# Optimization experiments

Hardware: AMD Instinct MI355X
Metric: run time of the kernel (lower is better)

## Reference

```python
import jax, jax.numpy as jnp
import numpy as np

DIM = 2048
DIM_VISUAL = 1024
HEADS = 16
DIM_HEAD = 64
INNER = HEADS * DIM_HEAD  # 1024
EPS = 1e-5


def setup_inputs() -> dict:
    key = jax.random.key(0)
    ks = jax.random.split(key, 6)
    y = jax.random.normal(ks[0], (4, 2048, DIM), dtype=jnp.float32)
    visual_features = jax.random.normal(ks[1], (4, 8, 64, DIM_VISUAL), dtype=jnp.float32)
    ln_g = jnp.ones((DIM,), dtype=jnp.float32)
    ln_b = jnp.zeros((DIM,), dtype=jnp.float32)
    Wq = jax.random.normal(ks[2], (DIM, INNER), dtype=jnp.float32) * 0.02
    Wkv = jax.random.normal(ks[3], (DIM_VISUAL, 2 * INNER), dtype=jnp.float32) * 0.02
    Wo = jax.random.normal(ks[4], (INNER, DIM), dtype=jnp.float32) * 0.02
    return {"y": y, "visual_features": visual_features, "ln_g": ln_g, "ln_b": ln_b,
            "Wq": Wq, "Wkv": Wkv, "Wo": Wo}


def reference(y, visual_features, ln_g, ln_b, Wq, Wkv, Wo):
    scale = DIM_HEAD ** (-0.5)
    b, t, nq, dv = visual_features.shape
    # LayerNorm over last dim
    mu = jnp.mean(y, axis=-1, keepdims=True)
    var = jnp.mean(jnp.square(y - mu), axis=-1, keepdims=True)
    yn = (y - mu) * jax.lax.rsqrt(var + EPS) * ln_g + ln_b
    q = (yn @ Wq) * scale                      # (b, n, inner)
    vis = visual_features.reshape(b, t * nq, dv)
    kv = vis @ Wkv                             # (b, m, 2*inner)
    k, v = jnp.split(kv, 2, axis=-1)
    # split heads: b n (h d) -> b h n d
    split = lambda x: x.reshape(x.shape[0], x.shape[1], HEADS, DIM_HEAD).transpose(0, 2, 1, 3)
    q, k, v = split(q), split(k), split(v)
    sim = jnp.einsum('bhid,bhjd->bhij', q, k)
    alphas = jax.nn.softmax(sim, axis=-1)      # amax-subtract softmax (stable)
    out = jnp.einsum('bhij,bhjd->bhid', alphas, v)
    out = out.transpose(0, 2, 1, 3).reshape(out.shape[0], out.shape[2], INNER)
    return out @ Wo
```

## Files before the change

### kernel.cpp

```cpp
#include <hip/hip_runtime.h>
#include <stdint.h>

typedef unsigned short u16;
typedef __bf16 bfrag __attribute__((ext_vector_type(8)));
typedef float f32x4 __attribute__((ext_vector_type(4)));
typedef u16 u16x4 __attribute__((ext_vector_type(4)));

__device__ __forceinline__ float bf2f(u16 u) {
  union { unsigned i; float f; } x; x.i = ((unsigned)u) << 16; return x.f;
}
__device__ __forceinline__ u16 f2bf(float f) {
  union { unsigned i; float f; } x; x.f = f;
  unsigned r = x.i + 0x7fffu + ((x.i >> 16) & 1u);
  return (u16)(r >> 16);
}
__device__ __forceinline__ unsigned packbf(float lo, float hi) {
  return (unsigned)f2bf(lo) | ((unsigned)f2bf(hi) << 16);
}

__device__ __forceinline__ f32x4 mfma16(bfrag a, bfrag b, f32x4 c) {
  return __builtin_amdgcn_mfma_f32_16x16x32_bf16(a, b, c, 0, 0, 0);
}

__device__ __forceinline__ void gl_lds16(const u16* g, const u16* l) {
  __builtin_amdgcn_global_load_lds(
      (const __attribute__((address_space(1))) unsigned int*)g,
      (__attribute__((address_space(3))) unsigned int*)l, 16, 0, 0);
}

__device__ __forceinline__ void xcd_swizzle(int& bx, int& by) {
  int gx = gridDim.x, nwg = gx * gridDim.y;
  int flat = by * gx + bx;
  int cpx = nwg >> 3;
  int swz = (flat & 7) * cpx + (flat >> 3);
  bx = swz % gx;
  by = swz / gx;
}

__global__ __launch_bounds__(256) void k_transpose(const float* __restrict__ in,
                                                   u16* __restrict__ out, int R, int C) {
  __shared__ u16 tile[32][33];
  int c0 = blockIdx.x * 32, r0 = blockIdx.y * 32;
  int tx = threadIdx.x, ty = threadIdx.y;
#pragma unroll
  for (int i = 0; i < 4; ++i)
    tile[ty + i * 8][tx] = f2bf(in[(size_t)(r0 + ty + i * 8) * C + c0 + tx]);
  __syncthreads();
#pragma unroll
  for (int i = 0; i < 4; ++i)
    out[(size_t)(c0 + ty + i * 8) * R + r0 + tx] = tile[tx][ty + i * 8];
}

__global__ __launch_bounds__(256) void k_cast(const float* __restrict__ in,
                                              u16* __restrict__ out, int n8) {
  int i = blockIdx.x * 256 + threadIdx.x;
  if (i >= n8) return;
  float4 a = *(const float4*)(in + (size_t)i * 8);
  float4 b = *(const float4*)(in + (size_t)i * 8 + 4);
  uint4 ov; u16* po = (u16*)&ov;
  po[0] = f2bf(a.x); po[1] = f2bf(a.y); po[2] = f2bf(a.z); po[3] = f2bf(a.w);
  po[4] = f2bf(b.x); po[5] = f2bf(b.y); po[6] = f2bf(b.z); po[7] = f2bf(b.w);
  *(uint4*)(out + (size_t)i * 8) = ov;
}

__global__ __launch_bounds__(256) void k_layernorm(const float* __restrict__ y,
                                                   const float* __restrict__ g,
                                                   const float* __restrict__ bb,
                                                   u16* __restrict__ yn) {
  int row = blockIdx.x, t = threadIdx.x;
  const float* yr = y + (size_t)row * 2048 + t * 8;
  float4 v0 = *(const float4*)(yr);
  float4 v1 = *(const float4*)(yr + 4);
  float x[8] = {v0.x, v0.y, v0.z, v0.w, v1.x, v1.y, v1.z, v1.w};
  float s = 0.f, ss = 0.f;
#pragma unroll
  for (int j = 0; j < 8; ++j) { s += x[j]; ss += x[j] * x[j]; }
#pragma unroll
  for (int off = 32; off > 0; off >>= 1) {
    s += __shfl_down(s, off);
    ss += __shfl_down(ss, off);
  }
  __shared__ float rs[4], rq[4];
  int lane = t & 63, wid = t >> 6;
  if (lane == 0) { rs[wid] = s; rq[wid] = ss; }
  __syncthreads();
  float S = rs[0] + rs[1] + rs[2] + rs[3];
  float Q = rq[0] + rq[1] + rq[2] + rq[3];
  float mean = S * (1.f / 2048.f);
  float var = Q * (1.f / 2048.f) - mean * mean;
  float rstd = rsqrtf(var + 1e-5f);
  float4 g0 = *(const float4*)(g + t * 8);
  float4 g1 = *(const float4*)(g + t * 8 + 4);
  float4 b0 = *(const float4*)(bb + t * 8);
  float4 b1 = *(const float4*)(bb + t * 8 + 4);
  float gg[8] = {g0.x, g0.y, g0.z, g0.w, g1.x, g1.y, g1.z, g1.w};
  float bv[8] = {b0.x, b0.y, b0.z, b0.w, b1.x, b1.y, b1.z, b1.w};
  uint4 ov; u16* po = (u16*)&ov;
#pragma unroll
  for (int j = 0; j < 8; ++j)
    po[j] = f2bf((x[j] - mean) * rstd * gg[j] + bv[j]);
  *(uint4*)(yn + (size_t)row * 2048 + t * 8) = ov;
}

template <bool F32OUT>
__global__ __launch_bounds__(256) void k_gemm_bt(const u16* __restrict__ A,
                                                 const u16* __restrict__ Bt,
                                                 void* __restrict__ Cv,
                                                 int M, int N, int K, float scale) {
  __shared__ __align__(16) u16 As[128 * 64];
  __shared__ __align__(16) u16 Bs[128 * 64];
  int t = threadIdx.x, lane = t & 63, wid = t >> 6;
  int wm = wid >> 1, wn = wid & 1;
  int bx = blockIdx.x, by = blockIdx.y;
  xcd_swizzle(bx, by);
  int m0 = by * 128, n0 = bx * 128;
  int lr = lane & 15, lg = lane >> 4;
  int sk = lr & 7;

  f32x4 acc[4][4];
#pragma unroll
  for (int i = 0; i < 4; ++i)
#pragma unroll
    for (int j = 0; j < 4; ++j) acc[i][j] = (f32x4){0.f, 0.f, 0.f, 0.f};

  int srow[4], scol[4], sbase[4];
#pragma unroll
  for (int j = 0; j < 4; ++j) {
    int s0 = (wid * 4 + j) * 64;
    int s = s0 + lane;
    srow[j] = s >> 3;
    scol[j] = ((s & 7) ^ (srow[j] & 7)) * 8;
    sbase[j] = s0 * 8;
  }

  for (int k0 = 0; k0 < K; k0 += 64) {
#pragma unroll
    for (int j = 0; j < 4; ++j) {
      gl_lds16(A + (size_t)(m0 + srow[j]) * K + k0 + scol[j], As + sbase[j]);
      gl_lds16(Bt + (size_t)(n0 + srow[j]) * K + k0 + scol[j], Bs + sbase[j]);
    }
    __syncthreads();
#pragma unroll
    for (int kk = 0; kk < 2; ++kk) {
      bfrag a[4], b[4];
#pragma unroll
      for (int i = 0; i < 4; ++i)
        a[i] = *(const bfrag*)(As + (wm * 64 + i * 16 + lr) * 64 + (((kk * 4 + lg) ^ sk) * 8));
#pragma unroll
      for (int j = 0; j < 4; ++j)
        b[j] = *(const bfrag*)(Bs + (wn * 64 + j * 16 + lr) * 64 + (((kk * 4 + lg) ^ sk) * 8));
#pragma unroll
      for (int i = 0; i < 4; ++i)
#pragma unroll
        for (int j = 0; j < 4; ++j)
          acc[i][j] = mfma16(a[i], b[j], acc[i][j]);
    }
    __syncthreads();
  }
#pragma unroll
  for (int i = 0; i < 4; ++i)
#pragma unroll
    for (int j = 0; j < 4; ++j) {
      int r0 = m0 + wm * 64 + i * 16 + lg * 4;
      int c0 = n0 + wn * 64 + j * 16 + lr;
#pragma unroll
      for (int r = 0; r < 4; ++r) {
        float v = scale * acc[i][j][r];
        if (F32OUT)
          ((float*)Cv)[(size_t)(r0 + r) * N + c0] = v;
        else
          ((u16*)Cv)[(size_t)(r0 + r) * N + c0] = f2bf(v);
      }
    }
}

__global__ __launch_bounds__(256) void k_gemm_kv(const u16* __restrict__ A,
                                                 const u16* __restrict__ Bt,
                                                 u16* __restrict__ Kb,
                                                 u16* __restrict__ Vtb) {
  const int K = 1024;
  __shared__ __align__(16) u16 As[128 * 64];
  __shared__ __align__(16) u16 Bs[128 * 64];
  int t = threadIdx.x, lane = t & 63, wid = t >> 6;
  int wm = wid >> 1, wn = wid & 1;
  int bx = blockIdx.x, by = blockIdx.y;
  xcd_swizzle(bx, by);
  int m0 = by * 128, n0 = bx * 128;
  int lr = lane & 15, lg = lane >> 4;
  int sk = lr & 7;

  f32x4 acc[4][4];
#pragma unroll
  for (int i = 0; i < 4; ++i)
#pragma unroll
    for (int j = 0; j < 4; ++j) acc[i][j] = (f32x4){0.f, 0.f, 0.f, 0.f};

  int srow[4], scol[4], sbase[4];
#pragma unroll
  for (int j = 0; j < 4; ++j) {
    int s0 = (wid * 4 + j) * 64;
    int s = s0 + lane;
    srow[j] = s >> 3;
    scol[j] = ((s & 7) ^ (srow[j] & 7)) * 8;
    sbase[j] = s0 * 8;
  }

  for (int k0 = 0; k0 < K; k0 += 64) {
#pragma unroll
    for (int j = 0; j < 4; ++j) {
      gl_lds16(A + (size_t)(m0 + srow[j]) * K + k0 + scol[j], As + sbase[j]);
      gl_lds16(Bt + (size_t)(n0 + srow[j]) * K + k0 + scol[j], Bs + sbase[j]);
    }
    __syncthreads();
#pragma unroll
    for (int kk = 0; kk < 2; ++kk) {
      bfrag a[4], b[4];
#pragma unroll
      for (int i = 0; i < 4; ++i)
        a[i] = *(const bfrag*)(As + (wm * 64 + i * 16 + lr) * 64 + (((kk * 4 + lg) ^ sk) * 8));
#pragma unroll
      for (int j = 0; j < 4; ++j)
        b[j] = *(const bfrag*)(Bs + (wn * 64 + j * 16 + lr) * 64 + (((kk * 4 + lg) ^ sk) * 8));
#pragma unroll
      for (int i = 0; i < 4; ++i)
#pragma unroll
        for (int j = 0; j < 4; ++j)
          acc[i][j] = mfma16(a[i], b[j], acc[i][j]);
    }
    __syncthreads();
  }
#pragma unroll
  for (int i = 0; i < 4; ++i)
#pragma unroll
    for (int j = 0; j < 4; ++j) {
      int r0 = m0 + wm * 64 + i * 16 + lg * 4;
      int c0 = n0 + wn * 64 + j * 16 + lr;
      if (c0 < 1024) {
#pragma unroll
        for (int r = 0; r < 4; ++r)
          Kb[(size_t)(r0 + r) * 1024 + c0] = f2bf(acc[i][j][r]);
      } else {
        int d = c0 - 1024;
        int hh = d >> 6, dd = d & 63;
        int bq = r0 >> 9, kvp = r0 & 511;
        u16x4 pk;
#pragma unroll
        for (int r = 0; r < 4; ++r) pk[r] = f2bf(acc[i][j][r]);
        *(u16x4*)(Vtb + ((size_t)(bq * 16 + hh) * 64 + dd) * 512 + kvp) = pk;
      }
    }
}

__global__ __launch_bounds__(256, 2) void k_attn(const u16* __restrict__ q,
                                                 const u16* __restrict__ kb,
                                                 const u16* __restrict__ vt,
                                                 u16* __restrict__ ao) {
  __shared__ __align__(16) u16 Ks[128 * 64];
  __shared__ __align__(16) u16 Vt[64 * 128];
  int t = threadIdx.x, lane = t & 63, wid = t >> 6;
  int lr = lane & 15, lg = lane >> 4;
  int sk = lr & 7;
  int a_ = lg >> 1, b_ = lg & 1;
  int bh = blockIdx.y, b = bh >> 4, h = bh & 15;
  int q0 = blockIdx.x * 128 + wid * 32;

  const u16* qg = q + (size_t)(b * 2048 + q0) * 1024 + h * 64;
  bfrag qf[2][2];
#pragma unroll
  for (int rt = 0; rt < 2; ++rt)
#pragma unroll
    for (int kk = 0; kk < 2; ++kk)
      qf[rt][kk] = *(const bfrag*)(qg + (size_t)(rt * 16 + lr) * 1024 + kk * 32 + lg * 8);

  f32x4 o[2][4];
#pragma unroll
  for (int rt = 0; rt < 2; ++rt)
#pragma unroll
    for (int dt = 0; dt < 4; ++dt) o[rt][dt] = (f32x4){0.f, 0.f, 0.f, 0.f};
  float m_s[2] = {-1e30f, -1e30f}, l_s[2] = {0.f, 0.f};

  const u16* kgb = kb + (size_t)(b * 512) * 1024 + h * 64;
  const u16* vgb = vt + (size_t)bh * 64 * 512;

  int krow[4], kcol[4], kbase[4];
#pragma unroll
  for (int j = 0; j < 4; ++j) {
    int g = wid * 4 + j;
    int s = g * 64 + lane;
    krow[j] = s >> 3;
    kcol[j] = ((s & 7) ^ (krow[j] & 7)) * 8;
    kbase[j] = g * 512;
  }

  for (int it = 0; it < 4; ++it) {
    int kv0 = it * 128;
#pragma unroll
    for (int j = 0; j < 4; ++j)
      gl_lds16(kgb + (size_t)(kv0 + krow[j]) * 1024 + kcol[j], Ks + kbase[j]);
#pragma unroll
    for (int j = 0; j < 4; ++j) {
      int g = wid * 4 + j;
      int d = g * 4 + (lane >> 4);
      int p = lane & 15;
      gl_lds16(vgb + (size_t)d * 512 + kv0 + ((p ^ (d & 7)) * 8), Vt + g * 512);
    }
    __syncthreads();

#pragma unroll
    for (int rt = 0; rt < 2; ++rt) {
      f32x4 s[8];
#pragma unroll
      for (int ct = 0; ct < 8; ++ct) {
        s[ct] = (f32x4){0.f, 0.f, 0.f, 0.f};
#pragma unroll
        for (int kk = 0; kk < 2; ++kk) {
          bfrag kf = *(const bfrag*)(Ks + (ct * 16 + lr) * 64 + (((kk * 4 + lg) ^ sk) * 8));
          s[ct] = mfma16(kf, qf[rt][kk], s[ct]);
        }
      }
      float mloc = -1e30f;
#pragma unroll
      for (int ct = 0; ct < 8; ++ct)
#pragma unroll
        for (int r = 0; r < 4; ++r) mloc = fmaxf(mloc, s[ct][r]);
      mloc = fmaxf(mloc, __shfl_xor(mloc, 16));
      mloc = fmaxf(mloc, __shfl_xor(mloc, 32));
      float mn = fmaxf(m_s[rt], mloc);
      float scq = __expf(m_s[rt] - mn);
      float ps = 0.f;
#pragma unroll
      for (int ct = 0; ct < 8; ++ct)
#pragma unroll
        for (int r = 0; r < 4; ++r) {
          float p = __expf(s[ct][r] - mn);
          s[ct][r] = p;
          ps += p;
        }
      ps += __shfl_xor(ps, 16);
      ps += __shfl_xor(ps, 32);
      l_s[rt] = l_s[rt] * scq + ps;
      m_s[rt] = mn;
      float sc4[4];
#pragma unroll
      for (int r = 0; r < 4; ++r) sc4[r] = __shfl(scq, (lane & 48) | (lg * 4 + r));
#pragma unroll
      for (int dt = 0; dt < 4; ++dt)
#pragma unroll
        for (int r = 0; r < 4; ++r) o[rt][dt][r] *= sc4[r];

      unsigned w0[8], w1[8];
#pragma unroll
      for (int ct = 0; ct < 8; ++ct) {
        w0[ct] = packbf(s[ct][0], s[ct][1]);
        w1[ct] = packbf(s[ct][2], s[ct][3]);
      }
      bfrag pf[4];
#pragma unroll
      for (int kt = 0; kt < 4; ++kt) {
        unsigned c0w0 = w0[2 * kt], c0w1 = w1[2 * kt];
        unsigned c1w0 = w0[2 * kt + 1], c1w1 = w1[2 * kt + 1];
        unsigned s0 = a_ ? c0w0 : c1w0;
        unsigned s1 = a_ ? c0w1 : c1w1;
        unsigned k0 = a_ ? c1w0 : c0w0;
        unsigned k1 = a_ ? c1w1 : c0w1;
        unsigned r0 = (unsigned)__shfl_xor((int)s0, 32);
        unsigned r1 = (unsigned)__shfl_xor((int)s1, 32);
        unsigned x0 = (a_ == b_) ? r0 : k0;
        unsigned x1 = (a_ == b_) ? r1 : k1;
        unsigned kk0 = (a_ == b_) ? k0 : r0;
        unsigned kk1 = (a_ == b_) ? k1 : r1;
        unsigned q0_ = (unsigned)__shfl_xor((int)x0, 16);
        unsigned q1_ = (unsigned)__shfl_xor((int)x1, 16);
        union { unsigned u[4]; bfrag f; } uf;
        uf.u[0] = b_ ? q0_ : kk0;
        uf.u[1] = b_ ? q1_ : kk1;
        uf.u[2] = b_ ? kk0 : q0_;
        uf.u[3] = b_ ? kk1 : q1_;
        pf[kt] = uf.f;
      }
#pragma unroll
      for (int dt = 0; dt < 4; ++dt)
#pragma unroll
        for (int kt = 0; kt < 4; ++kt) {
          int d = dt * 16 + lr;
          bfrag vfb = *(const bfrag*)(Vt + d * 128 + (((kt * 4 + lg) ^ (d & 7)) * 8));
          o[rt][dt] = mfma16(pf[kt], vfb, o[rt][dt]);
        }
    }
    __syncthreads();
  }

#pragma unroll
  for (int rt = 0; rt < 2; ++rt) {
    float invq = 1.f / l_s[rt];
    float i4[4];
#pragma unroll
    for (int r = 0; r < 4; ++r) i4[r] = __shfl(invq, (lane & 48) | (lg * 4 + r));
#pragma unroll
    for (int dt = 0; dt < 4; ++dt)
#pragma unroll
      for (int r = 0; r < 4; ++r)
        ao[(size_t)(b * 2048 + q0 + rt * 16 + lg * 4 + r) * 1024 + h * 64 + dt * 16 + lr] =
            f2bf(o[rt][dt][r] * i4[r]);
  }
}

extern "C" void kernel_launch(void* const* d_in, const int* in_sizes, int n_in,
                              void* d_out, int out_size, void* d_ws, size_t ws_size,
                              hipStream_t stream) {
  const float* y   = (const float*)d_in[0];
  const float* vf  = (const float*)d_in[1];
  const float* g   = (const float*)d_in[2];
  const float* bb  = (const float*)d_in[3];
  const float* Wq  = (const float*)d_in[4];
  const float* Wkv = (const float*)d_in[5];
  const float* Wo  = (const float*)d_in[6];
  float* out = (float*)d_out;
  char* ws = (char*)d_ws;

  u16* qb   = (u16*)(ws + 0ull);
  u16* kbuf = (u16*)(ws + 16777216ull);
  u16* vtb  = (u16*)(ws + 20971520ull);
  u16* aob  = (u16*)(ws + 25165824ull);
  u16* wqT  = (u16*)(ws + 41943040ull);
  u16* wkvT = (u16*)(ws + 46137344ull);
  u16* woT  = (u16*)(ws + 50331648ull);
  u16* vfb  = (u16*)(ws + 54525952ull);
  u16* yn = (u16*)d_out;

  dim3 tb(32, 8, 1);
  k_transpose<<<dim3(1024 / 32, 2048 / 32, 1), tb, 0, stream>>>(Wq, wqT, 2048, 1024);
  k_transpose<<<dim3(2048 / 32, 1024 / 32, 1), tb, 0, stream>>>(Wkv, wkvT, 1024, 2048);
  k_transpose<<<dim3(2048 / 32, 1024 / 32, 1), tb, 0, stream>>>(Wo, woT, 1024, 2048);
  k_cast<<<(2048 * 1024 / 8 + 255) / 256, 256, 0, stream>>>(vf, vfb, 2048 * 1024 / 8);
  k_layernorm<<<8192, 256, 0, stream>>>(y, g, bb, yn);
  k_gemm_bt<false><<<dim3(1024 / 128, 8192 / 128, 1), 256, 0, stream>>>(yn, wqT, qb, 8192, 1024, 2048, 0.125f);
  k_gemm_kv<<<dim3(2048 / 128, 2048 / 128, 1), 256, 0, stream>>>(vfb, wkvT, kbuf, vtb);
  k_attn<<<dim3(16, 64, 1), 256, 0, stream>>>(qb, kbuf, vtb, aob);
  k_gemm_bt<true><<<dim3(2048 / 128, 8192 / 128, 1), 256, 0, stream>>>(aob, woT, out, 8192, 2048, 1024, 1.0f);
}
```

Before: 189.2 us.

## Double-buffer LDS tiles in GEMM and attention kernels to overlap loads

Adds a second LDS buffer for the A/B tiles in both GEMM kernels and for the K/V tiles in the attention kernel. The next tile's global-to-LDS copy is issued before computing on the current tile, with one barrier per iteration. The aim is to hide global load latency behind the MFMA work. It doubles LDS use per block (64KB for the GEMMs, 64KB for attention at 2 blocks/CU), which may reduce occupancy. The loop now has a single barrier per step, so correctness depends on gl_lds16 completion being covered by __syncthreads.

```diff
diff --git a/kernel.cpp b/kernel.cpp
--- a/kernel.cpp
+++ b/kernel.cpp
@@ -107,8 +107,8 @@
                                                  const u16* __restrict__ Bt,
                                                  void* __restrict__ Cv,
                                                  int M, int N, int K, float scale) {
-  __shared__ __align__(16) u16 As[128 * 64];
-  __shared__ __align__(16) u16 Bs[128 * 64];
+  __shared__ __align__(16) u16 As[2][128 * 64];
+  __shared__ __align__(16) u16 Bs[2][128 * 64];
   int t = threadIdx.x, lane = t & 63, wid = t >> 6;
   int wm = wid >> 1, wn = wid & 1;
   int bx = blockIdx.x, by = blockIdx.y;
@@ -133,29 +133,42 @@
     sbase[j] = s0 * 8;
   }
 
-  for (int k0 = 0; k0 < K; k0 += 64) {
-#pragma unroll
-    for (int j = 0; j < 4; ++j) {
-      gl_lds16(A + (size_t)(m0 + srow[j]) * K + k0 + scol[j], As + sbase[j]);
-      gl_lds16(Bt + (size_t)(n0 + srow[j]) * K + k0 + scol[j], Bs + sbase[j]);
-    }
-    __syncthreads();
+#pragma unroll
+  for (int j = 0; j < 4; ++j) {
+    gl_lds16(A + (size_t)(m0 + srow[j]) * K + scol[j], As[0] + sbase[j]);
+    gl_lds16(Bt + (size_t)(n0 + srow[j]) * K + scol[j], Bs[0] + sbase[j]);
+  }
+  __syncthreads();
+
+  int nk = K >> 6;
+  for (int kt = 0; kt < nk; ++kt) {
+    int cur = kt & 1;
+    if (kt + 1 < nk) {
+      int k0 = (kt + 1) << 6;
+#pragma unroll
+      for (int j = 0; j < 4; ++j) {
+        gl_lds16(A + (size_t)(m0 + srow[j]) * K + k0 + scol[j], As[cur ^ 1] + sbase[j]);
+        gl_lds16(Bt + (size_t)(n0 + srow[j]) * K + k0 + scol[j], Bs[cur ^ 1] + sbase[j]);
+      }
+    }
+    const u16* as = As[cur];
+    const u16* bs = Bs[cur];
 #pragma unroll
     for (int kk = 0; kk < 2; ++kk) {
       bfrag a[4], b[4];
 #pragma unroll
       for (int i = 0; i < 4; ++i)
-        a[i] = *(const bfrag*)(As + (wm * 64 + i * 16 + lr) * 64 + (((kk * 4 + lg) ^ sk) * 8));
+        a[i] = *(const bfrag*)(as + (wm * 64 + i * 16 + lr) * 64 + (((kk * 4 + lg) ^ sk) * 8));
 #pragma unroll
       for (int j = 0; j < 4; ++j)
-        b[j] = *(const bfrag*)(Bs + (wn * 64 + j * 16 + lr) * 64 + (((kk * 4 + lg) ^ sk) * 8));
+        b[j] = *(const bfrag*)(bs + (wn * 64 + j * 16 + lr) * 64 + (((kk * 4 + lg) ^ sk) * 8));
 #pragma unroll
       for (int i = 0; i < 4; ++i)
 #pragma unroll
         for (int j = 0; j < 4; ++j)
           acc[i][j] = mfma16(a[i], b[j], acc[i][j]);
     }
-    __syncthreads();
+    if (kt + 1 < nk) __syncthreads();
   }
 #pragma unroll
   for (int i = 0; i < 4; ++i)
@@ -179,8 +192,8 @@
                                                  u16* __restrict__ Kb,
                                                  u16* __restrict__ Vtb) {
   const int K = 1024;
-  __shared__ __align__(16) u16 As[128 * 64];
-  __shared__ __align__(16) u16 Bs[128 * 64];
+  __shared__ __align__(16) u16 As[2][128 * 64];
+  __shared__ __align__(16) u16 Bs[2][128 * 64];
   int t = threadIdx.x, lane = t & 63, wid = t >> 6;
   int wm = wid >> 1, wn = wid & 1;
   int bx = blockIdx.x, by = blockIdx.y;
@@ -205,29 +218,42 @@
     sbase[j] = s0 * 8;
   }
 
-  for (int k0 = 0; k0 < K; k0 += 64) {
-#pragma unroll
-    for (int j = 0; j < 4; ++j) {
-      gl_lds16(A + (size_t)(m0 + srow[j]) * K + k0 + scol[j], As + sbase[j]);
-      gl_lds16(Bt + (size_t)(n0 + srow[j]) * K + k0 + scol[j], Bs + sbase[j]);
-    }
-    __syncthreads();
+#pragma unroll
+  for (int j = 0; j < 4; ++j) {
+    gl_lds16(A + (size_t)(m0 + srow[j]) * K + scol[j], As[0] + sbase[j]);
+    gl_lds16(Bt + (size_t)(n0 + srow[j]) * K + scol[j], Bs[0] + sbase[j]);
+  }
+  __syncthreads();
+
+  int nk = K >> 6;
+  for (int kt = 0; kt < nk; ++kt) {
+    int cur = kt & 1;
+    if (kt + 1 < nk) {
+      int k0 = (kt + 1) << 6;
+#pragma unroll
+      for (int j = 0; j < 4; ++j) {
+        gl_lds16(A + (size_t)(m0 + srow[j]) * K + k0 + scol[j], As[cur ^ 1] + sbase[j]);
+        gl_lds16(Bt + (size_t)(n0 + srow[j]) * K + k0 + scol[j], Bs[cur ^ 1] + sbase[j]);
+      }
+    }
+    const u16* as = As[cur];
+    const u16* bs = Bs[cur];
 #pragma unroll
     for (int kk = 0; kk < 2; ++kk) {
       bfrag a[4], b[4];
 #pragma unroll
       for (int i = 0; i < 4; ++i)
-        a[i] = *(const bfrag*)(As + (wm * 64 + i * 16 + lr) * 64 + (((kk * 4 + lg) ^ sk) * 8));
+        a[i] = *(const bfrag*)(as + (wm * 64 + i * 16 + lr) * 64 + (((kk * 4 + lg) ^ sk) * 8));
 #pragma unroll
       for (int j = 0; j < 4; ++j)
-        b[j] = *(const bfrag*)(Bs + (wn * 64 + j * 16 + lr) * 64 + (((kk * 4 + lg) ^ sk) * 8));
+        b[j] = *(const bfrag*)(bs + (wn * 64 + j * 16 + lr) * 64 + (((kk * 4 + lg) ^ sk) * 8));
 #pragma unroll
       for (int i = 0; i < 4; ++i)
 #pragma unroll
         for (int j = 0; j < 4; ++j)
           acc[i][j] = mfma16(a[i], b[j], acc[i][j]);
     }
-    __syncthreads();
+    if (kt + 1 < nk) __syncthreads();
   }
 #pragma unroll
   for (int i = 0; i < 4; ++i)
@@ -255,8 +281,8 @@
                                                  const u16* __restrict__ kb,
                                                  const u16* __restrict__ vt,
                                                  u16* __restrict__ ao) {
-  __shared__ __align__(16) u16 Ks[128 * 64];
-  __shared__ __align__(16) u16 Vt[64 * 128];
+  __shared__ __align__(16) u16 Ks[2][128 * 64];
+  __shared__ __align__(16) u16 Vt[2][64 * 128];
   int t = threadIdx.x, lane = t & 63, wid = t >> 6;
   int lr = lane & 15, lg = lane >> 4;
   int sk = lr & 7;
@@ -291,20 +317,37 @@
     kcol[j] = ((s & 7) ^ (krow[j] & 7)) * 8;
     kbase[j] = g * 512;
   }
+  int vd = (threadIdx.x >> 4) & 3;
+
+#pragma unroll
+  for (int j = 0; j < 4; ++j)
+    gl_lds16(kgb + (size_t)krow[j] * 1024 + kcol[j], Ks[0] + kbase[j]);
+#pragma unroll
+  for (int j = 0; j < 4; ++j) {
+    int g = wid * 4 + j;
+    int d = g * 4 + (lane >> 4);
+    int p = lane & 15;
+    gl_lds16(vgb + (size_t)d * 512 + ((p ^ (d & 7)) * 8), Vt[0] + g * 512);
+  }
+  __syncthreads();
 
   for (int it = 0; it < 4; ++it) {
-    int kv0 = it * 128;
-#pragma unroll
-    for (int j = 0; j < 4; ++j)
-      gl_lds16(kgb + (size_t)(kv0 + krow[j]) * 1024 + kcol[j], Ks + kbase[j]);
-#pragma unroll
-    for (int j = 0; j < 4; ++j) {
-      int g = wid * 4 + j;
-      int d = g * 4 + (lane >> 4);
-      int p = lane & 15;
-      gl_lds16(vgb + (size_t)d * 512 + kv0 + ((p ^ (d & 7)) * 8), Vt + g * 512);
-    }
-    __syncthreads();
+    int cur = it & 1;
+    if (it + 1 < 4) {
+      int kv1 = (it + 1) * 128;
+#pragma unroll
+      for (int j = 0; j < 4; ++j)
+        gl_lds16(kgb + (size_t)(kv1 + krow[j]) * 1024 + kcol[j], Ks[cur ^ 1] + kbase[j]);
+#pragma unroll
+      for (int j = 0; j < 4; ++j) {
+        int g = wid * 4 + j;
+        int d = g * 4 + (lane >> 4);
+        int p = lane & 15;
+        gl_lds16(vgb + (size_t)d * 512 + kv1 + ((p ^ (d & 7)) * 8), Vt[cur ^ 1] + g * 512);
+      }
+    }
+    const u16* ks = Ks[cur];
+    const u16* vtl = Vt[cur];
 
 #pragma unroll
     for (int rt = 0; rt < 2; ++rt) {
@@ -314,7 +357,7 @@
         s[ct] = (f32x4){0.f, 0.f, 0.f, 0.f};
 #pragma unroll
         for (int kk = 0; kk < 2; ++kk) {
-          bfrag kf = *(const bfrag*)(Ks + (ct * 16 + lr) * 64 + (((kk * 4 + lg) ^ sk) * 8));
+          bfrag kf = *(const bfrag*)(ks + (ct * 16 + lr) * 64 + (((kk * 4 + lg) ^ sk) * 8));
           s[ct] = mfma16(kf, qf[rt][kk], s[ct]);
         }
       }
@@ -383,11 +426,11 @@
 #pragma unroll
         for (int kt = 0; kt < 4; ++kt) {
           int d = dt * 16 + lr;
-          bfrag vfb = *(const bfrag*)(Vt + d * 128 + (((kt * 4 + lg) ^ (d & 7)) * 8));
+          bfrag vfb = *(const bfrag*)(vtl + d * 128 + (((kt * 4 + lg) ^ (d & 7)) * 8));
           o[rt][dt] = mfma16(pf[kt], vfb, o[rt][dt]);
         }
     }
-    __syncthreads();
+    if (it + 1 < 4) __syncthreads();
   }
 
 #pragma unroll
```

After: 178.1 us. 5.8% less time.
